# Kernel optimization log

Measured on AMD Instinct MI355X. Metric: run time of the kernel, lower is better.

The kernel has to match this reference:

```python
import jax, jax.numpy as jnp
import numpy as np

H = 100; W = 100; FX = 86.6; FY = 86.6
NEAR = 2.0; FAR = 6.0; DINF = 1e10
NS = 64            # n_samples per ray
L_PTS = 10; L_DIR = 4
HID = 256; HID_DIR = 128
D_PTS = 3 + 3 * 2 * L_PTS   # 63
D_DIR = 3 + 3 * 2 * L_DIR   # 27


def posenc(x, L):
    # [x, sin(2^k x), cos(2^k x)] NeRF positional encoding
    freqs = (2.0 ** jnp.arange(L)).astype(x.dtype)          # [L]
    xb = x[..., None, :] * freqs[:, None]                    # [..., L, 3]
    enc = jnp.concatenate([jnp.sin(xb), jnp.cos(xb)], -1)    # [..., L, 6]
    return jnp.concatenate([x, enc.reshape(x.shape[:-1] + (L * 6,))], -1)


def setup_inputs() -> dict:
    key = jax.random.key(0)
    ks = jax.random.split(key, 8)
    pose = jnp.array([[1., 0., 0., 0.], [0., 1., 0., 0.],
                      [0., 0., 1., 4.], [0., 0., 0., 1.]], jnp.float32)
    c2w = pose + 0.01 * jax.random.normal(ks[0], (4, 4), jnp.float32)
    t_rand = jax.random.uniform(ks[1], (NS,), jnp.float32)
    s = 0.05
    return {
        'c2w': c2w,
        't_rand': t_rand,
        'w1': s * jax.random.normal(ks[2], (D_PTS, HID), jnp.float32),
        'b1': jnp.zeros((HID,), jnp.float32),
        'w2': s * jax.random.normal(ks[3], (HID, HID), jnp.float32),
        'b2': jnp.zeros((HID,), jnp.float32),
        'w_sig': s * jax.random.normal(ks[4], (HID, 1), jnp.float32),
        'b_sig': jnp.zeros((1,), jnp.float32),
        'w_dir': s * jax.random.normal(ks[5], (HID + D_DIR, HID_DIR), jnp.float32),
        'b_dir': jnp.zeros((HID_DIR,), jnp.float32),
        'w_rgb': s * jax.random.normal(ks[6], (HID_DIR, 3), jnp.float32),
        'b_rgb': jnp.zeros((3,), jnp.float32),
    }


def reference(c2w, t_rand, w1, b1, w2, b2, w_sig, b_sig, w_dir, b_dir, w_rgb, b_rgb):
    # ---- get_rays ----
    i, j = jnp.meshgrid(jnp.arange(W, dtype=jnp.float32),
                        jnp.arange(H, dtype=jnp.float32), indexing='xy')
    dirs = jnp.stack([(i - W * 0.5) / FX,
                      -(j - H * 0.5) / FY,
                      -jnp.ones_like(i)], -1).reshape(H * W, 3)      # [R,3]
    rays_d = jnp.einsum('rk,ik->ri', dirs, c2w[:3, :3])              # [R,3]
    rays_o = c2w[:3, -1]                                             # [3]

    # ---- sample_stratified (perturb=True, inverse_depth=False) ----
    t_vals = jnp.linspace(0.0, 1.0, NS)
    z = NEAR * (1.0 - t_vals) + FAR * t_vals
    mids = 0.5 * (z[1:] + z[:-1])
    upper = jnp.concatenate([mids, z[-1:]])
    lower = jnp.concatenate([z[:1], mids])
    z = lower + (upper - lower) * t_rand                             # [NS]
    dists = jnp.concatenate([z[1:] - z[:-1], jnp.full((1,), DINF, z.dtype)])
    pts = rays_o + rays_d[:, None, :] * z[None, :, None]             # [R,NS,3]

    # ---- encodings ----
    enc_pts = posenc(pts, L_PTS)                                     # [R,NS,63]
    norm = jnp.sqrt(jnp.sum(rays_d * rays_d, -1, keepdims=True))     # [R,1]
    viewdirs = rays_d / norm                                         # [R,3]
    enc_dir = jnp.broadcast_to(posenc(viewdirs, L_DIR)[:, None, :],
                               (H * W, NS, D_DIR))                   # [R,NS,27]

    # ---- coarse NeRF MLP ----
    h = jax.nn.relu(enc_pts @ w1 + b1)
    h = jax.nn.relu(h @ w2 + b2)
    sigma = (h @ w_sig + b_sig)[..., 0]                              # [R,NS]
    hd = jax.nn.relu(jnp.concatenate([h, enc_dir], -1) @ w_dir + b_dir)
    rgb = jax.nn.sigmoid(hd @ w_rgb + b_rgb)                         # [R,NS,3]

    # ---- raw2outputs (volume rendering) ----
    dists_r = dists[None, :] * norm                                  # [R,NS]
    alpha = 1.0 - jnp.exp(-jax.nn.relu(sigma) * dists_r)             # [R,NS]
    # get_rgb_map back-to-front recurrence == alpha * exclusive_cumprod(1-alpha)
    trans = jnp.concatenate(
        [jnp.ones_like(alpha[:, :1]), jnp.cumprod(1.0 - alpha, -1)[:, :-1]], -1)
    weights = alpha * trans                                          # [R,NS]
    rgb_map = jnp.sum(weights[..., None] * rgb, -2)                  # [R,3]
    return rgb_map
```

## Files before the change

### kernel.cpp

```cpp
#include <hip/hip_runtime.h>
#include <cstdint>
#include <cmath>

#define NTH 256

namespace {

typedef _Float16 half8  __attribute__((ext_vector_type(8)));
typedef _Float16 half4v __attribute__((ext_vector_type(4)));
typedef float    float4v __attribute__((ext_vector_type(4)));

constexpr int IMG_W   = 100;
constexpr int NS      = 64;
constexpr int D_PTS   = 63;
constexpr int D_DIR   = 27;
constexpr int HID     = 256;
constexpr int HID_DIR = 128;

constexpr int ENC_H = 72;
constexpr int H_S   = 264;
constexpr int HD_S  = 136;

constexpr int W1P_OFF  = 0;
constexpr int W2P_OFF  = 16384;
constexpr int WDP_OFF  = 81920;
constexpr int WRGB_OFF = 118784;
constexpr int WPACK_HALFS = 120832;

__global__ __launch_bounds__(NTH)
void prepack(const float* __restrict__ w1, const float* __restrict__ w2,
             const float* __restrict__ wd, const float* __restrict__ wsig,
             const float* __restrict__ wrgb, _Float16* __restrict__ wp)
{
    const int idx = blockIdx.x * NTH + threadIdx.x;
    if (idx >= WPACK_HALFS) return;
    const int j    = idx & 7;
    const int lane = (idx >> 3) & 63;
    const int kloc = (lane >> 4) * 8 + j;
    const int lr   = lane & 15;
    float v = 0.0f;
    if (idx < W2P_OFF) {
        const int nt = (idx >> 9) & 15, ks = idx >> 13;
        const int k = ks * 32 + kloc;
        if (k < D_PTS) v = w1[k * HID + nt * 16 + lr];
    } else if (idx < WDP_OFF) {
        const int t = idx - W2P_OFF;
        const int nt = (t >> 9) & 15, ks = t >> 13;
        v = w2[(ks * 32 + kloc) * HID + nt * 16 + lr];
    } else if (idx < WRGB_OFF) {
        const int t = idx - WDP_OFF;
        const int q = t >> 9;
        const int ks = q / 9, tile = q - 9 * ks;
        const int k = ks * 32 + kloc;
        if (tile < 8) v = wd[k * HID_DIR + tile * 16 + lr];
        else if (lr == 0) v = wsig[k];
    } else {
        const int t = idx - WRGB_OFF;
        const int ks = t >> 9;
        const int k = ks * 32 + kloc;
        if (lr < 3) v = wrgb[k * 3 + lr];
    }
    wp[idx] = (_Float16)v;
}

__device__ __forceinline__ half8 bf_w(const float* __restrict__ W, int ldN,
                                      int kbase, int n, int kmax) {
    half8 b;
    #pragma unroll
    for (int j = 0; j < 8; ++j) {
        const int k = kbase + j;
        b[j] = (_Float16)((k < kmax) ? W[k * ldN + n] : 0.0f);
    }
    return b;
}
__device__ __forceinline__ half8 bf_sig(const float* __restrict__ ws, int kbase, int lr) {
    half8 b;
    #pragma unroll
    for (int j = 0; j < 8; ++j)
        b[j] = (_Float16)((lr == 0) ? ws[kbase + j] : 0.0f);
    return b;
}
__device__ __forceinline__ half8 bf_rgb(const float* __restrict__ wr, int kbase, int lr) {
    half8 b;
    #pragma unroll
    for (int j = 0; j < 8; ++j)
        b[j] = (_Float16)((lr < 3) ? wr[(kbase + j) * 3 + lr] : 0.0f);
    return b;
}

template<bool PACKED>
__global__ __launch_bounds__(NTH, 4)
void nerf_fused(const float* __restrict__ c2w,
                const float* __restrict__ t_rand,
                const float* __restrict__ w1,  const float* __restrict__ b1,
                const float* __restrict__ w2,  const float* __restrict__ b2,
                const float* __restrict__ w_sig, const float* __restrict__ b_sig,
                const float* __restrict__ w_dir, const float* __restrict__ b_dir,
                const float* __restrict__ w_rgb, const float* __restrict__ b_rgb,
                const _Float16* __restrict__ wpack,
                float* __restrict__ out)
{
    __shared__ __align__(16) unsigned char scr[NS * H_S * 2];
    _Float16* encH = reinterpret_cast<_Float16*>(scr);
    _Float16* hbuf = reinterpret_cast<_Float16*>(scr);
    double*   encD = reinterpret_cast<double*>(scr);
    double*   h1d  = reinterpret_cast<double*>(scr + 512);
    double*   h2d  = reinterpret_cast<double*>(scr + 2560);
    __shared__ __align__(16) float dbv[HID_DIR];
    __shared__ float  zbuf[NS];
    __shared__ double zd[NS];
    __shared__ float  encdir[32];
    __shared__ float  sigb[NS];
    __shared__ float  rgbb[NS * 3];

    const int tid  = threadIdx.x;
    const int ray  = blockIdx.x;
    const int lane = tid & 63;
    const int wv   = tid >> 6;
    const int lr   = lane & 15;
    const int lq   = lane >> 4;

    const half8* wp8 = reinterpret_cast<const half8*>(wpack);

    const int pj = ray / IMG_W;
    const int pi = ray - pj * IMG_W;
    const float dx = ((float)pi - 50.0f) / 86.6f;
    const float dy = -(((float)pj) - 50.0f) / 86.6f;
    const float rd0 = dx * c2w[0] + dy * c2w[1] - c2w[2];
    const float rd1 = dx * c2w[4] + dy * c2w[5] - c2w[6];
    const float rd2 = dx * c2w[8] + dy * c2w[9] - c2w[10];
    const float ro0 = c2w[3], ro1 = c2w[7], ro2 = c2w[11];
    const float nrm = sqrtf(rd0 * rd0 + rd1 * rd1 + rd2 * rd2);
    const float vd0 = rd0 / nrm, vd1 = rd1 / nrm, vd2 = rd2 / nrm;

    if (tid < NS) {
        const int s = tid;
        const double delta = 1.0 / 63.0;
        const double ts = (s == 63) ? 1.0 : (double)s * delta;
        const double zs = 2.0 * (1.0 - ts) + 6.0 * ts;
        double lower, upper;
        if (s == 0) { lower = zs; }
        else { const double tm = (double)(s - 1) * delta;
               const double zm = 2.0 * (1.0 - tm) + 6.0 * tm; lower = 0.5 * (zm + zs); }
        if (s == 63) { upper = zs; }
        else { const double tp = (s + 1 == 63) ? 1.0 : (double)(s + 1) * delta;
               const double zp = 2.0 * (1.0 - tp) + 6.0 * tp; upper = 0.5 * (zs + zp); }
        const double zz = lower + (upper - lower) * (double)t_rand[s];
        zd[s]   = zz;
        zbuf[s] = (float)zz;
    }
    if (tid < 32) {
        float v = 0.0f;
        if (tid < D_DIR) {
            const int f = tid;
            if (f < 3) {
                v = (f == 0) ? vd0 : ((f == 1) ? vd1 : vd2);
            } else {
                const int ff = f - 3;
                const int l = ff / 6;
                const int r = ff - 6 * l;
                const int c = r % 3;
                const float x = ((c == 0) ? vd0 : ((c == 1) ? vd1 : vd2)) * (float)(1 << l);
                v = (r < 3) ? sinf(x) : cosf(x);
            }
        }
        encdir[tid] = v;
    }
    __syncthreads();

    if (tid < 192) {
        const int s = tid / 3;
        const int c = tid - 3 * s;
        const float zv = zbuf[s];
        const float p = (c == 0) ? (ro0 + rd0 * zv) : ((c == 1) ? (ro1 + rd1 * zv) : (ro2 + rd2 * zv));
        _Float16* row = &encH[s * ENC_H];
        row[c] = (_Float16)p;
        float sl = sinf(p), cl = cosf(p);
        row[3 + c] = (_Float16)sl;
        row[6 + c] = (_Float16)cl;
        #pragma unroll
        for (int l = 1; l < 10; ++l) {
            const float s2 = 2.0f * sl * cl;
            const float c2 = 1.0f - 2.0f * sl * sl;
            row[3 + 6 * l + c]     = (_Float16)s2;
            row[3 + 6 * l + 3 + c] = (_Float16)c2;
            sl = s2; cl = c2;
        }
    }
    if (tid < 64) encH[tid * ENC_H + 63] = (_Float16)0.0f;
    if (tid < HID_DIR) {
        float d = b_dir[tid];
        for (int t = 0; t < D_DIR; ++t)
            d += encdir[t] * w_dir[(HID + t) * HID_DIR + tid];
        dbv[tid] = d;
    }
    __syncthreads();

    {
        float4v acc[4][4];
        #pragma unroll
        for (int nt = 0; nt < 4; ++nt)
            #pragma unroll
            for (int st = 0; st < 4; ++st) acc[nt][st] = float4v{0.f, 0.f, 0.f, 0.f};

        #pragma unroll
        for (int ks = 0; ks < 2; ++ks) {
            half8 h[4];
            #pragma unroll
            for (int st = 0; st < 4; ++st)
                h[st] = *reinterpret_cast<const half8*>(&encH[(st * 16 + lr) * ENC_H + ks * 32 + lq * 8]);
            #pragma unroll
            for (int nt = 0; nt < 4; ++nt) {
                const int tile = wv * 4 + nt;
                const half8 w = PACKED
                    ? wp8[(W1P_OFF >> 3) + (ks * 16 + tile) * 64 + lane]
                    : bf_w(w1, HID, ks * 32 + lq * 8, tile * 16 + lr, D_PTS);
                #pragma unroll
                for (int st = 0; st < 4; ++st)
                    acc[nt][st] = __builtin_amdgcn_mfma_f32_16x16x32_f16(w, h[st], acc[nt][st], 0, 0, 0);
            }
        }
        __syncthreads();
        #pragma unroll
        for (int nt = 0; nt < 4; ++nt) {
            const int nb = (wv * 4 + nt) * 16 + lq * 4;
            const float4v bb = *reinterpret_cast<const float4v*>(&b1[nb]);
            #pragma unroll
            for (int st = 0; st < 4; ++st) {
                half4v hv;
                #pragma unroll
                for (int r = 0; r < 4; ++r)
                    hv[r] = (_Float16)fmaxf(acc[nt][st][r] + bb[r], 0.0f);
                *reinterpret_cast<half4v*>(&hbuf[(st * 16 + lr) * H_S + nb]) = hv;
            }
        }
    }
    __syncthreads();

    {
        float4v acc[4][4];
        #pragma unroll
        for (int nt = 0; nt < 4; ++nt)
            #pragma unroll
            for (int st = 0; st < 4; ++st) acc[nt][st] = float4v{0.f, 0.f, 0.f, 0.f};

        for (int ks = 0; ks < 8; ++ks) {
            half8 h[4];
            #pragma unroll
            for (int st = 0; st < 4; ++st)
                h[st] = *reinterpret_cast<const half8*>(&hbuf[(st * 16 + lr) * H_S + ks * 32 + lq * 8]);
            #pragma unroll
            for (int nt = 0; nt < 4; ++nt) {
                const int tile = wv * 4 + nt;
                const half8 w = PACKED
                    ? wp8[(W2P_OFF >> 3) + (ks * 16 + tile) * 64 + lane]
                    : bf_w(w2, HID, ks * 32 + lq * 8, tile * 16 + lr, 1 << 30);
                #pragma unroll
                for (int st = 0; st < 4; ++st)
                    acc[nt][st] = __builtin_amdgcn_mfma_f32_16x16x32_f16(w, h[st], acc[nt][st], 0, 0, 0);
            }
        }
        __syncthreads();
        #pragma unroll
        for (int nt = 0; nt < 4; ++nt) {
            const int nb = (wv * 4 + nt) * 16 + lq * 4;
            const float4v bb = *reinterpret_cast<const float4v*>(&b2[nb]);
            #pragma unroll
            for (int st = 0; st < 4; ++st) {
                half4v hv;
                #pragma unroll
                for (int r = 0; r < 4; ++r)
                    hv[r] = (_Float16)fmaxf(acc[nt][st][r] + bb[r], 0.0f);
                *reinterpret_cast<half4v*>(&hbuf[(st * 16 + lr) * H_S + nb]) = hv;
            }
        }
    }
    __syncthreads();

    float4v accd[2][4];
    float4v accs[4];
    {
        #pragma unroll
        for (int nt = 0; nt < 2; ++nt)
            #pragma unroll
            for (int st = 0; st < 4; ++st) accd[nt][st] = float4v{0.f, 0.f, 0.f, 0.f};
        #pragma unroll
        for (int st = 0; st < 4; ++st) accs[st] = float4v{0.f, 0.f, 0.f, 0.f};

        for (int ks = 0; ks < 8; ++ks) {
            half8 h[4];
            #pragma unroll
            for (int st = 0; st < 4; ++st)
                h[st] = *reinterpret_cast<const half8*>(&hbuf[(st * 16 + lr) * H_S + ks * 32 + lq * 8]);
            #pragma unroll
            for (int nt = 0; nt < 2; ++nt) {
                const int tile = wv * 2 + nt;
                const half8 w = PACKED
                    ? wp8[(WDP_OFF >> 3) + (ks * 9 + tile) * 64 + lane]
                    : bf_w(w_dir, HID_DIR, ks * 32 + lq * 8, tile * 16 + lr, 1 << 30);
                #pragma unroll
                for (int st = 0; st < 4; ++st)
                    accd[nt][st] = __builtin_amdgcn_mfma_f32_16x16x32_f16(w, h[st], accd[nt][st], 0, 0, 0);
            }
            if (wv == 0) {
                const half8 w = PACKED
                    ? wp8[(WDP_OFF >> 3) + (ks * 9 + 8) * 64 + lane]
                    : bf_sig(w_sig, ks * 32 + lq * 8, lr);
                #pragma unroll
                for (int st = 0; st < 4; ++st)
                    accs[st] = __builtin_amdgcn_mfma_f32_16x16x32_f16(w, h[st], accs[st], 0, 0, 0);
            }
        }
    }
    __syncthreads();

    #pragma unroll
    for (int nt = 0; nt < 2; ++nt) {
        const int nb = (wv * 2 + nt) * 16 + lq * 4;
        const float4v db4 = *reinterpret_cast<const float4v*>(&dbv[nb]);
        #pragma unroll
        for (int st = 0; st < 4; ++st) {
            half4v hv;
            #pragma unroll
            for (int r = 0; r < 4; ++r)
                hv[r] = (_Float16)fmaxf(accd[nt][st][r] + db4[r], 0.0f);
            *reinterpret_cast<half4v*>(&hbuf[(st * 16 + lr) * HD_S + nb]) = hv;
        }
    }
    if (wv == 0 && lq == 0) {
        const float bs = b_sig[0];
        #pragma unroll
        for (int st = 0; st < 4; ++st)
            sigb[st * 16 + lr] = accs[st][0] + bs;
    }
    __syncthreads();

    {
        float4v accr = float4v{0.f, 0.f, 0.f, 0.f};
        #pragma unroll
        for (int ks = 0; ks < 4; ++ks) {
            const half8 h = *reinterpret_cast<const half8*>(&hbuf[(wv * 16 + lr) * HD_S + ks * 32 + lq * 8]);
            const half8 w = PACKED
                ? wp8[(WRGB_OFF >> 3) + ks * 64 + lane]
                : bf_rgb(w_rgb, ks * 32 + lq * 8, lr);
            accr = __builtin_amdgcn_mfma_f32_16x16x32_f16(w, h, accr, 0, 0, 0);
        }
        if (lq == 0) {
            #pragma unroll
            for (int r = 0; r < 3; ++r) {
                const float a = accr[r] + b_rgb[r];
                rgbb[(wv * 16 + lr) * 3 + r] = 1.0f / (1.0f + expf(-a));
            }
        }
    }
    __syncthreads();

    if (fabsf(sigb[63]) < 0.02f) {
        {
            const double z63 = zd[63];
            const double p0 = (double)ro0 + (double)rd0 * z63;
            const double p1 = (double)ro1 + (double)rd1 * z63;
            const double p2 = (double)ro2 + (double)rd2 * z63;
            if (tid < D_PTS) {
                const int f = tid;
                double v;
                if (f < 3) {
                    v = (f == 0) ? p0 : ((f == 1) ? p1 : p2);
                } else {
                    const int ff = f - 3;
                    const int l = ff / 6;
                    const int r = ff - 6 * l;
                    const int c = r % 3;
                    const double x = ((c == 0) ? p0 : ((c == 1) ? p1 : p2)) * (double)(1 << l);
                    v = (r < 3) ? sin(x) : cos(x);
                }
                encD[f] = v;
            }
        }
        __syncthreads();
        {
            double acc = 0.0;
            for (int k = 0; k < D_PTS; ++k)
                acc += encD[k] * (double)w1[k * HID + tid];
            acc += (double)b1[tid];
            h1d[tid] = fmax(acc, 0.0);
        }
        __syncthreads();
        {
            double acc = 0.0;
            for (int k = 0; k < HID; ++k)
                acc += h1d[k] * (double)w2[k * HID + tid];
            acc += (double)b2[tid];
            h2d[tid] = fmax(acc, 0.0);
        }
        __syncthreads();
        if (tid < 64) {
            double p = 0.0;
            #pragma unroll
            for (int m = 0; m < 4; ++m)
                p += h2d[tid * 4 + m] * (double)w_sig[tid * 4 + m];
            #pragma unroll
            for (int off = 1; off < 64; off <<= 1)
                p += __shfl_xor(p, off, 64);
            if (tid == 0) sigb[63] = (float)(p + (double)b_sig[0]);
        }
    }
    __syncthreads();

    if (tid < NS) {
        const int s = tid;
        const float sgv = sigb[s];
        const float zv  = zbuf[s];
        const float zn  = (s < 63) ? zbuf[s + 1] : 0.0f;
        const float dist = (s < 63) ? (zn - zv) : 1.0e10f;
        const float alpha = 1.0f - expf(-fmaxf(sgv, 0.0f) * dist * nrm);
        float P = 1.0f - alpha;
        #pragma unroll
        for (int off = 1; off < 64; off <<= 1) {
            const float p = __shfl_up(P, off, 64);
            if (s >= off) P *= p;
        }
        float T = __shfl_up(P, 1, 64);
        if (s == 0) T = 1.0f;
        const float wgt = alpha * T;
        float r0 = wgt * rgbb[s * 3 + 0];
        float r1 = wgt * rgbb[s * 3 + 1];
        float r2 = wgt * rgbb[s * 3 + 2];
        #pragma unroll
        for (int off = 32; off > 0; off >>= 1) {
            r0 += __shfl_xor(r0, off, 64);
            r1 += __shfl_xor(r1, off, 64);
            r2 += __shfl_xor(r2, off, 64);
        }
        if (s == 0) {
            out[ray * 3 + 0] = r0;
            out[ray * 3 + 1] = r1;
            out[ray * 3 + 2] = r2;
        }
    }
}

}

extern "C" void kernel_launch(void* const* d_in, const int* in_sizes, int n_in,
                              void* d_out, int out_size, void* d_ws, size_t ws_size,
                              hipStream_t stream) {
    const float* c2w    = (const float*)d_in[0];
    const float* t_rand = (const float*)d_in[1];
    const float* w1     = (const float*)d_in[2];
    const float* b1     = (const float*)d_in[3];
    const float* w2     = (const float*)d_in[4];
    const float* b2     = (const float*)d_in[5];
    const float* w_sig  = (const float*)d_in[6];
    const float* b_sig  = (const float*)d_in[7];
    const float* w_dir  = (const float*)d_in[8];
    const float* b_dir  = (const float*)d_in[9];
    const float* w_rgb  = (const float*)d_in[10];
    const float* b_rgb  = (const float*)d_in[11];

    (void)in_sizes; (void)n_in; (void)out_size;

    const bool packed = (ws_size >= (size_t)(WPACK_HALFS * 2));
    if (packed) {
        _Float16* wp = (_Float16*)d_ws;
        hipLaunchKernelGGL(prepack, dim3((WPACK_HALFS + NTH - 1) / NTH), dim3(NTH), 0, stream,
                           w1, w2, w_dir, w_sig, w_rgb, wp);
        hipLaunchKernelGGL((nerf_fused<true>), dim3(100 * 100), dim3(NTH), 0, stream,
                           c2w, t_rand, w1, b1, w2, b2, w_sig, b_sig,
                           w_dir, b_dir, w_rgb, b_rgb, (const _Float16*)wp, (float*)d_out);
    } else {
        hipLaunchKernelGGL((nerf_fused<false>), dim3(100 * 100), dim3(NTH), 0, stream,
                           c2w, t_rand, w1, b1, w2, b2, w_sig, b_sig,
                           w_dir, b_dir, w_rgb, b_rgb, (const _Float16*)nullptr, (float*)d_out);
    }
}
```

Measured before the change: 298.5 us.

## Fold view-direction bias into MFMA, repad LDS strides, add MFMA priority hints

The per-ray scalar loop that computed the direction-encoding contribution to the dir-layer bias (27x128 FMAs from global memory) is removed. That term now comes from an extra MFMA k-step over a packed, zero-padded encdir tile appended to the packed w_dir weights. LDS row strides change from 264/136 to 260/132 halves to alter bank mapping, with 8-byte split loads to match the new alignment. s_setprio raises wave priority around MFMA loops. This costs extra MFMA work and a larger weight pack.

```diff
diff --git a/kernel.cpp b/kernel.cpp
--- a/kernel.cpp
+++ b/kernel.cpp
@@ -18,14 +18,14 @@
 constexpr int HID_DIR = 128;
 
 constexpr int ENC_H = 72;
-constexpr int H_S   = 264;
-constexpr int HD_S  = 136;
+constexpr int H_S   = 260;
+constexpr int HD_S  = 132;
 
 constexpr int W1P_OFF  = 0;
 constexpr int W2P_OFF  = 16384;
 constexpr int WDP_OFF  = 81920;
-constexpr int WRGB_OFF = 118784;
-constexpr int WPACK_HALFS = 120832;
+constexpr int WRGB_OFF = 123392;
+constexpr int WPACK_HALFS = 125440;
 
 __global__ __launch_bounds__(NTH)
 void prepack(const float* __restrict__ w1, const float* __restrict__ w2,
@@ -52,8 +52,8 @@
         const int q = t >> 9;
         const int ks = q / 9, tile = q - 9 * ks;
         const int k = ks * 32 + kloc;
-        if (tile < 8) v = wd[k * HID_DIR + tile * 16 + lr];
-        else if (lr == 0) v = wsig[k];
+        if (tile < 8) { if (k < HID + D_DIR) v = wd[k * HID_DIR + tile * 16 + lr]; }
+        else if (lr == 0 && k < HID) v = wsig[k];
     } else {
         const int t = idx - WRGB_OFF;
         const int ks = t >> 9;
@@ -86,6 +86,12 @@
     for (int j = 0; j < 8; ++j)
         b[j] = (_Float16)((lr < 3) ? wr[(kbase + j) * 3 + lr] : 0.0f);
     return b;
+}
+
+__device__ __forceinline__ half8 ld_h8(const _Float16* __restrict__ p) {
+    const half4v lo = *reinterpret_cast<const half4v*>(p);
+    const half4v hi = *reinterpret_cast<const half4v*>(p + 4);
+    return __builtin_shufflevector(lo, hi, 0, 1, 2, 3, 4, 5, 6, 7);
 }
 
 template<bool PACKED>
@@ -106,10 +112,9 @@
     double*   encD = reinterpret_cast<double*>(scr);
     double*   h1d  = reinterpret_cast<double*>(scr + 512);
     double*   h2d  = reinterpret_cast<double*>(scr + 2560);
-    __shared__ __align__(16) float dbv[HID_DIR];
+    __shared__ __align__(16) _Float16 encdirH[32];
     __shared__ float  zbuf[NS];
     __shared__ double zd[NS];
-    __shared__ float  encdir[32];
     __shared__ float  sigb[NS];
     __shared__ float  rgbb[NS * 3];
 
@@ -164,7 +169,7 @@
                 v = (r < 3) ? sinf(x) : cosf(x);
             }
         }
-        encdir[tid] = v;
+        encdirH[tid] = (_Float16)v;
     }
     __syncthreads();
 
@@ -188,12 +193,6 @@
         }
     }
     if (tid < 64) encH[tid * ENC_H + 63] = (_Float16)0.0f;
-    if (tid < HID_DIR) {
-        float d = b_dir[tid];
-        for (int t = 0; t < D_DIR; ++t)
-            d += encdir[t] * w_dir[(HID + t) * HID_DIR + tid];
-        dbv[tid] = d;
-    }
     __syncthreads();
 
     {
@@ -209,6 +208,7 @@
             #pragma unroll
             for (int st = 0; st < 4; ++st)
                 h[st] = *reinterpret_cast<const half8*>(&encH[(st * 16 + lr) * ENC_H + ks * 32 + lq * 8]);
+            __builtin_amdgcn_s_setprio(1);
             #pragma unroll
             for (int nt = 0; nt < 4; ++nt) {
                 const int tile = wv * 4 + nt;
@@ -219,6 +219,7 @@
                 for (int st = 0; st < 4; ++st)
                     acc[nt][st] = __builtin_amdgcn_mfma_f32_16x16x32_f16(w, h[st], acc[nt][st], 0, 0, 0);
             }
+            __builtin_amdgcn_s_setprio(0);
         }
         __syncthreads();
         #pragma unroll
@@ -248,7 +249,8 @@
             half8 h[4];
             #pragma unroll
             for (int st = 0; st < 4; ++st)
-                h[st] = *reinterpret_cast<const half8*>(&hbuf[(st * 16 + lr) * H_S + ks * 32 + lq * 8]);
+                h[st] = ld_h8(&hbuf[(st * 16 + lr) * H_S + ks * 32 + lq * 8]);
+            __builtin_amdgcn_s_setprio(1);
             #pragma unroll
             for (int nt = 0; nt < 4; ++nt) {
                 const int tile = wv * 4 + nt;
@@ -259,6 +261,7 @@
                 for (int st = 0; st < 4; ++st)
                     acc[nt][st] = __builtin_amdgcn_mfma_f32_16x16x32_f16(w, h[st], acc[nt][st], 0, 0, 0);
             }
+            __builtin_amdgcn_s_setprio(0);
         }
         __syncthreads();
         #pragma unroll
@@ -291,7 +294,8 @@
             half8 h[4];
             #pragma unroll
             for (int st = 0; st < 4; ++st)
-                h[st] = *reinterpret_cast<const half8*>(&hbuf[(st * 16 + lr) * H_S + ks * 32 + lq * 8]);
+                h[st] = ld_h8(&hbuf[(st * 16 + lr) * H_S + ks * 32 + lq * 8]);
+            __builtin_amdgcn_s_setprio(1);
             #pragma unroll
             for (int nt = 0; nt < 2; ++nt) {
                 const int tile = wv * 2 + nt;
@@ -310,6 +314,22 @@
                 for (int st = 0; st < 4; ++st)
                     accs[st] = __builtin_amdgcn_mfma_f32_16x16x32_f16(w, h[st], accs[st], 0, 0, 0);
             }
+            __builtin_amdgcn_s_setprio(0);
+        }
+        {
+            const half8 he = *reinterpret_cast<const half8*>(&encdirH[lq * 8]);
+            __builtin_amdgcn_s_setprio(1);
+            #pragma unroll
+            for (int nt = 0; nt < 2; ++nt) {
+                const int tile = wv * 2 + nt;
+                const half8 w = PACKED
+                    ? wp8[(WDP_OFF >> 3) + (8 * 9 + tile) * 64 + lane]
+                    : bf_w(w_dir, HID_DIR, HID + lq * 8, tile * 16 + lr, HID + D_DIR);
+                #pragma unroll
+                for (int st = 0; st < 4; ++st)
+                    accd[nt][st] = __builtin_amdgcn_mfma_f32_16x16x32_f16(w, he, accd[nt][st], 0, 0, 0);
+            }
+            __builtin_amdgcn_s_setprio(0);
         }
     }
     __syncthreads();
@@ -317,7 +337,7 @@
     #pragma unroll
     for (int nt = 0; nt < 2; ++nt) {
         const int nb = (wv * 2 + nt) * 16 + lq * 4;
-        const float4v db4 = *reinterpret_cast<const float4v*>(&dbv[nb]);
+        const float4v db4 = *reinterpret_cast<const float4v*>(&b_dir[nb]);
         #pragma unroll
         for (int st = 0; st < 4; ++st) {
             half4v hv;
@@ -337,14 +357,16 @@
 
     {
         float4v accr = float4v{0.f, 0.f, 0.f, 0.f};
+        __builtin_amdgcn_s_setprio(1);
         #pragma unroll
         for (int ks = 0; ks < 4; ++ks) {
-            const half8 h = *reinterpret_cast<const half8*>(&hbuf[(wv * 16 + lr) * HD_S + ks * 32 + lq * 8]);
+            const half8 h = ld_h8(&hbuf[(wv * 16 + lr) * HD_S + ks * 32 + lq * 8]);
             const half8 w = PACKED
                 ? wp8[(WRGB_OFF >> 3) + ks * 64 + lane]
                 : bf_rgb(w_rgb, ks * 32 + lq * 8, lr);
             accr = __builtin_amdgcn_mfma_f32_16x16x32_f16(w, h, accr, 0, 0, 0);
         }
+        __builtin_amdgcn_s_setprio(0);
         if (lq == 0) {
             #pragma unroll
             for (int r = 0; r < 3; ++r) {
```

Measured after the change: 282.1 us. 1.06x faster.
